# Kernel tuning notes

Hardware: AMD Instinct MI355X
Metric: run time of the kernel (lower is better)

Reference implementation:

```python
import jax, jax.numpy as jnp
import numpy as np

EM_DIM = 64
GROUP = 16
DIM_IN = 1024


def _position_embedding(boxes, part_boxes):
    # boxes: [N,4], part_boxes: [P,4] -> [N,P,EM_DIM]
    xmin, ymin, xmax, ymax = [boxes[:, i:i + 1] for i in range(4)]            # [N,1]
    pxmin, pymin, pxmax, pymax = [part_boxes[:, i:i + 1].T for i in range(4)]  # [1,P]
    bw = xmax - xmin + 1.0
    bh = ymax - ymin + 1.0
    pw = pxmax - pxmin + 1.0
    ph = pymax - pymin + 1.0
    cx = 0.5 * (xmin + xmax)
    cy = 0.5 * (ymin + ymax)
    pcx = 0.5 * (pxmin + pxmax)
    pcy = 0.5 * (pymin + pymax)
    dx = jnp.abs((cx - pcx) / bw)
    dy = jnp.abs((cy - pcy) / bh)
    dx = jnp.log(jnp.where(dx < 1e-3, 1e-3, dx))
    dy = jnp.log(jnp.where(dy < 1e-3, 1e-3, dy))
    dw = jnp.log(pw / bw)
    dh = jnp.log(ph / bh)
    pos = jnp.stack([dx, dy, dw, dh], axis=2)                                  # [N,P,4]
    em_range = jnp.arange(EM_DIM // 8, dtype=pos.dtype) / (EM_DIM // 8)        # [8]
    em_mat = jnp.power(jnp.asarray(1000.0, pos.dtype), em_range)               # [8]
    div = (100.0 * pos)[..., None] / em_mat                                    # [N,P,4,8]
    emb = jnp.concatenate([jnp.sin(div), jnp.cos(div)], axis=3)                # [N,P,4,16]
    return emb.reshape(pos.shape[0], pos.shape[1], EM_DIM)


def _single_relation(boxes, part_boxes, bf, pf, Wg_w, Wg_b, Wq_w, Wq_b, Wk_w, Wk_b, conv_w, conv_b):
    N = bf.shape[0]
    P = pf.shape[0]
    emb = _position_embedding(boxes, part_boxes)                               # [N,P,64]
    pos_feat = jax.nn.relu(emb @ Wg_w.T + Wg_b)                                # [N,P,G]
    att_weight = jnp.transpose(pos_feat, (0, 2, 1))                            # [N,G,P]
    q = (bf @ Wq_w.T + Wq_b).reshape(N, GROUP, EM_DIM)                         # [N,G,64]
    k = (pf @ Wk_w.T + Wk_b).reshape(P, GROUP, EM_DIM)                         # [P,G,64]
    att = jnp.einsum('ngd,pgd->ngp', q, k) * (1.0 / GROUP)                     # [N,G,P]
    att_weight = jnp.where(att_weight < 1e-6, 1e-6, att_weight)
    sm = jax.nn.softmax(jnp.log(att_weight) + att, axis=2)                     # [N,G,P]
    out = jnp.einsum('ngp,pc->ngc', sm, pf)                                    # [N,G,dim_in]
    # grouped 1x1 conv: group g maps dim_in channels -> EM_DIM channels
    w3 = conv_w.reshape(GROUP, EM_DIM, DIM_IN)
    rel = jnp.einsum('ngc,goc->ngo', out, w3).reshape(N, GROUP * EM_DIM) + conv_b
    return rel                                                                  # [N, G*EM_DIM]


def setup_inputs() -> dict:
    key = jax.random.key(0)
    ks = jax.random.split(key, 12)
    N_TOT, P_TOT = 2048, 2048

    def make_rois(k1, k2, n, n1):
        xy = jax.random.uniform(k1, (n, 2), jnp.float32) * 800.0
        wh = jax.random.uniform(k2, (n, 2), jnp.float32) * 200.0 + 16.0
        boxes = jnp.concatenate([xy, xy + wh], axis=1)
        idx = jnp.concatenate([jnp.zeros((n1, 1)), jnp.ones((n - n1, 1))], axis=0).astype(jnp.float32)
        return jnp.concatenate([idx, boxes], axis=1)

    rois = make_rois(ks[0], ks[1], N_TOT, 1024)
    part_rois = make_rois(ks[2], ks[3], P_TOT, 1024)
    box_feats = jax.random.normal(ks[4], (N_TOT, DIM_IN), jnp.float32)
    part_feats = jax.random.normal(ks[5], (P_TOT, DIM_IN), jnp.float32)
    xav_g = float(np.sqrt(6.0 / (EM_DIM + GROUP)))
    xav_qk = float(np.sqrt(6.0 / (DIM_IN + GROUP * EM_DIM)))
    Wg_w = jax.random.uniform(ks[6], (GROUP, EM_DIM), jnp.float32, -xav_g, xav_g)
    Wg_b = jnp.zeros((GROUP,), jnp.float32)
    Wq_w = jax.random.uniform(ks[7], (GROUP * EM_DIM, DIM_IN), jnp.float32, -xav_qk, xav_qk)
    Wq_b = jnp.zeros((GROUP * EM_DIM,), jnp.float32)
    Wk_w = jax.random.uniform(ks[8], (GROUP * EM_DIM, DIM_IN), jnp.float32, -xav_qk, xav_qk)
    Wk_b = jnp.zeros((GROUP * EM_DIM,), jnp.float32)
    conv_w = jax.random.normal(ks[9], (GROUP * EM_DIM, DIM_IN), jnp.float32) * 0.02
    conv_b = jnp.zeros((GROUP * EM_DIM,), jnp.float32)
    return {"rois": rois, "part_rois": part_rois, "box_feats": box_feats,
            "part_feats": part_feats, "Wg_w": Wg_w, "Wg_b": Wg_b,
            "Wq_w": Wq_w, "Wq_b": Wq_b, "Wk_w": Wk_w, "Wk_b": Wk_b,
            "conv_w": conv_w, "conv_b": conv_b, "n1_boxes": 1024, "n1_parts": 1024}


def reference(rois, part_rois, box_feats, part_feats, Wg_w, Wg_b, Wq_w, Wq_b,
              Wk_w, Wk_b, conv_w, conv_b, n1_boxes, n1_parts):
    boxes = rois[:, 1:5]
    part_boxes = part_rois[:, 1:5]
    params = (Wg_w, Wg_b, Wq_w, Wq_b, Wk_w, Wk_b, conv_w, conv_b)
    rel1 = _single_relation(boxes[:n1_boxes], part_boxes[:n1_parts],
                            box_feats[:n1_boxes], part_feats[:n1_parts], *params)
    rel2 = _single_relation(boxes[n1_boxes:], part_boxes[n1_parts:],
                            box_feats[n1_boxes:], part_feats[n1_parts:], *params)
    return jnp.concatenate([rel1, rel2], axis=0)  # [N_total, GROUP*EM_DIM]
```

## Files before the change

kernel.cpp:

```cpp
#include <hip/hip_runtime.h>

typedef unsigned short u16;
using short8  = __attribute__((ext_vector_type(8))) short;
using float4v = __attribute__((ext_vector_type(4))) float;

__device__ __forceinline__ u16 f2bf(float f) {
    union { float f; unsigned u; } v; v.f = f;
    unsigned r = (v.u + 0x7fff + ((v.u >> 16) & 1)) >> 16;
    return (u16)r;
}
__device__ __forceinline__ float bf2f(u16 h) {
    union { unsigned u; float f; } v; v.u = ((unsigned)h) << 16; return v.f;
}
__device__ __forceinline__ unsigned pkbf(float lo, float hi) {
    unsigned d;
    asm("v_cvt_pk_bf16_f32 %0, %1, %2" : "=v"(d) : "v"(lo), "v"(hi));
    return d;
}
__device__ __forceinline__ float sin_rev(float r) {
    float f, s;
    asm("v_fract_f32 %0, %1" : "=v"(f) : "v"(r));
    asm("v_sin_f32 %0, %1" : "=v"(s) : "v"(f));
    return s;
}
__device__ __forceinline__ void dma16(const void* g, void* l) {
    __builtin_amdgcn_global_load_lds((const __attribute__((address_space(1))) void*)g,
                                     (__attribute__((address_space(3))) void*)l, 16, 0, 0);
}

__device__ __forceinline__ void cvt4(const float* __restrict__ s, u16* __restrict__ o, int i) {
    float4 v = ((const float4*)s)[i];
    uint2 r; r.x = pkbf(v.x, v.y); r.y = pkbf(v.z, v.w);
    ((uint2*)o)[i] = r;
}

__global__ __launch_bounds__(256)
void cvt_all(const float* __restrict__ s0, const float* __restrict__ s1,
             const float* __restrict__ s2, const float* __restrict__ s3,
             const float* __restrict__ s4, const float* __restrict__ prois,
             u16* __restrict__ o0, u16* __restrict__ o1, u16* __restrict__ o2,
             u16* __restrict__ o3, u16* __restrict__ o4, float4* __restrict__ PD,
             int na4, int nb4, int nw4, int PT) {
    int i = blockIdx.x * 256 + threadIdx.x;
    if (i < na4) { cvt4(s0, o0, i); return; }
    i -= na4;
    if (i < nb4) { cvt4(s1, o1, i); return; }
    i -= nb4;
    if (i < nw4) { cvt4(s2, o2, i); return; }
    i -= nw4;
    if (i < nw4) { cvt4(s3, o3, i); return; }
    i -= nw4;
    if (i < nw4) { cvt4(s4, o4, i); return; }
    i -= nw4;
    if (i < PT) {
        const float* pr = prois + (size_t)i * 5;
        float pxmin = pr[1], pymin = pr[2], pxmax = pr[3], pymax = pr[4];
        PD[i] = make_float4(0.5f * (pxmin + pxmax), 0.5f * (pymin + pymax),
                            __logf(pxmax - pxmin + 1.0f), __logf(pymax - pymin + 1.0f));
    }
}

__global__ __launch_bounds__(256)
void proj_mfma(const u16* __restrict__ Ab, const u16* __restrict__ Pb,
               const u16* __restrict__ Wqb, const u16* __restrict__ Wkb,
               const u16* __restrict__ Cwb, const float* __restrict__ bq,
               const float* __restrict__ bk, u16* __restrict__ Qb,
               u16* __restrict__ Kb, u16* __restrict__ PVt, int PT) {
    __shared__ __align__(16) u16 As[128 * 64];
    __shared__ __align__(16) u16 Ws[64 * 64];
    __shared__ __align__(16) u16 Tr[128 * 68];

    const int z = blockIdx.z;
    const int m0 = blockIdx.y * 128, j0 = blockIdx.x * 64;
    const u16* A = (z == 0) ? Ab : Pb;
    const u16* W = (z == 0) ? Wqb : (z == 1 ? Wkb : Cwb);
    const int t = threadIdx.x;
    const int w = t >> 6, lane = t & 63;
    const int wm = w >> 1, wn = w & 1;
    const int lr = lane >> 3, lc = lane & 7, gch = lc ^ lr;
    const int fm = lane & 15, quad = lane >> 4;

    float4v zero4 = {0.f, 0.f, 0.f, 0.f};
    float4v acc[4][2];
#pragma unroll
    for (int i = 0; i < 4; ++i) { acc[i][0] = zero4; acc[i][1] = zero4; }

    for (int k0 = 0; k0 < 1024; k0 += 64) {
#pragma unroll
        for (int i = 0; i < 4; ++i) {
            int row = w * 32 + i * 8 + lr;
            dma16(A + (size_t)(m0 + row) * 1024 + k0 + gch * 8,
                  As + (w * 32 + i * 8) * 64 + lane * 8);
        }
#pragma unroll
        for (int i = 0; i < 2; ++i) {
            int row = w * 16 + i * 8 + lr;
            dma16(W + (size_t)(j0 + row) * 1024 + k0 + gch * 8,
                  Ws + (w * 16 + i * 8) * 64 + lane * 8);
        }
        __syncthreads();
#pragma unroll
        for (int ks = 0; ks < 2; ++ks) {
            int c = ks * 4 + quad;
            short8 af[4], bf[2];
#pragma unroll
            for (int i = 0; i < 4; ++i) {
                int ra = wm * 64 + i * 16 + fm;
                af[i] = *(const short8*)(As + ra * 64 + ((c ^ (ra & 7)) * 8));
            }
#pragma unroll
            for (int j = 0; j < 2; ++j) {
                int rb = wn * 32 + j * 16 + fm;
                bf[j] = *(const short8*)(Ws + rb * 64 + ((c ^ (rb & 7)) * 8));
            }
#pragma unroll
            for (int i = 0; i < 4; ++i)
#pragma unroll
                for (int j = 0; j < 2; ++j)
                    acc[i][j] = __builtin_amdgcn_mfma_f32_16x16x32_bf16(af[i], bf[j], acc[i][j], 0, 0, 0);
        }
        __syncthreads();
    }

    if (z < 2) {
        u16* O = z ? Kb : Qb;
        const float* bias = z ? bk : bq;
#pragma unroll
        for (int j = 0; j < 2; ++j) {
            int jl = wn * 32 + j * 16 + fm;
            float bb = bias[j0 + jl];
#pragma unroll
            for (int i = 0; i < 4; ++i) {
                int mlb = wm * 64 + i * 16 + quad * 4;
#pragma unroll
                for (int r = 0; r < 4; ++r)
                    Tr[(mlb + r) * 68 + jl] = f2bf(acc[i][j][r] + bb);
            }
        }
        __syncthreads();
#pragma unroll
        for (int i2 = 0; i2 < 4; ++i2) {
            int f = i2 * 2048 + t * 8;
            int ml = f >> 6, jl = f & 63;
            union { uint2 u2[2]; short8 s8; } uu;
            uu.u2[0] = *(const uint2*)(Tr + ml * 68 + jl);
            uu.u2[1] = *(const uint2*)(Tr + ml * 68 + jl + 4);
            *(short8*)(O + (size_t)(m0 + ml) * 1024 + j0 + jl) = uu.s8;
        }
    } else {
#pragma unroll
        for (int j = 0; j < 2; ++j) {
            int jl = wn * 32 + j * 16 + fm;
#pragma unroll
            for (int i = 0; i < 4; ++i) {
                int mlb = wm * 64 + i * 16 + quad * 4;
                uint2 pk;
                pk.x = pkbf(acc[i][j][0], acc[i][j][1]);
                pk.y = pkbf(acc[i][j][2], acc[i][j][3]);
                *(uint2*)(Tr + jl * 136 + mlb) = pk;
            }
        }
        __syncthreads();
#pragma unroll
        for (int i2 = 0; i2 < 4; ++i2) {
            int f = i2 * 2048 + t * 8;
            int jl = f >> 7, ml = f & 127;
            union { uint2 u2[2]; short8 s8; } uu;
            uu.u2[0] = *(const uint2*)(Tr + jl * 136 + ml);
            uu.u2[1] = *(const uint2*)(Tr + jl * 136 + ml + 4);
            *(short8*)(PVt + (size_t)(j0 + jl) * PT + m0 + ml) = uu.s8;
        }
    }
}

__global__ __launch_bounds__(256)
void posw_fused(const float* __restrict__ rois, const float4* __restrict__ PD,
                const float* __restrict__ Wg_w, const float* __restrict__ Wg_b,
                u16* __restrict__ POSW, const int* __restrict__ n1b_p,
                const int* __restrict__ n1p_p, int PT) {
    const int n = blockIdx.x, t = threadIdx.x;
    const int w = t >> 6, lane = t & 63;
    const int fm = lane & 15, quad = lane >> 4;
    const int n1b = *n1b_p, n1p = *n1p_p;
    const int hh = (n >= n1b) ? 1 : 0;
    const int p0 = hh ? n1p : 0;
    const int Ph = hh ? (PT - n1p) : n1p;

    float xmin = rois[n * 5 + 1], ymin = rois[n * 5 + 2];
    float xmax = rois[n * 5 + 3], ymax = rois[n * 5 + 4];
    float bw = xmax - xmin + 1.0f, bh = ymax - ymin + 1.0f;
    float cx = 0.5f * (xmin + xmax), cy = 0.5f * (ymin + ymax);

    const int jA = quad >> 1, trig = quad & 1;
    float cA   = (jA == 0) ? cx : cy;
    float invA = (jA == 0) ? (1.0f / bw) : (1.0f / bh);
    float lB   = (jA == 0) ? __logf(bw) : __logf(bh);
    float toff = trig ? 0.25f : 0.0f;

    const int g_ = fm;
    short8 b1, b2;
    {
        const float* w1 = Wg_w + g_ * 64 + quad * 8;
        const float* w2 = Wg_w + g_ * 64 + 32 + quad * 8;
        unsigned* p1 = (unsigned*)&b1;
        unsigned* p2 = (unsigned*)&b2;
#pragma unroll
        for (int kk = 0; kk < 4; ++kk) {
            p1[kk] = pkbf(w1[2 * kk], w1[2 * kk + 1]);
            p2[kk] = pkbf(w2[2 * kk], w2[2 * kk + 1]);
        }
    }
    float wgb = Wg_b[g_];

    const float inv_em[8] = {1.0f, 0.4216965034f, 0.1778279410f, 0.0749894209f,
                             0.0316227766f, 0.0133352143f, 0.0056234133f, 0.0023713737f};
    const float REV = 15.91549431f;
    const int prange = Ph >> 2;
    const int pb0 = w * prange;
    u16* rowp = POSW + ((size_t)n * 16 + g_) * 1024;

    float4 pd_c = PD[p0 + pb0 + fm];

#pragma unroll 2
    for (int pt = 0; pt < 16; ++pt) {
        int pbase = pb0 + pt * 16;
        float4 pd_n;
        if (pt < 15) pd_n = PD[p0 + pbase + 16 + fm];
        float pc = (jA == 0) ? pd_c.x : pd_c.y;
        float lp = (jA == 0) ? pd_c.z : pd_c.w;
        float posA = __logf(fmaxf(fabsf(cA - pc) * invA, 0.001f));
        float posB = lp - lB;
        float br1 = posA * REV, br2 = posB * REV;
        float e1[8], e2[8];
#pragma unroll
        for (int k = 0; k < 8; ++k) {
            e1[k] = sin_rev(fmaf(br1, inv_em[k], toff));
            e2[k] = sin_rev(fmaf(br2, inv_em[k], toff));
        }
        short8 a1, a2;
        unsigned* pa1 = (unsigned*)&a1;
        unsigned* pa2 = (unsigned*)&a2;
#pragma unroll
        for (int kk = 0; kk < 4; ++kk) {
            pa1[kk] = pkbf(e1[2 * kk], e1[2 * kk + 1]);
            pa2[kk] = pkbf(e2[2 * kk], e2[2 * kk + 1]);
        }
        float4v acc = {wgb, wgb, wgb, wgb};
        acc = __builtin_amdgcn_mfma_f32_16x16x32_bf16(a1, b1, acc, 0, 0, 0);
        acc = __builtin_amdgcn_mfma_f32_16x16x32_bf16(a2, b2, acc, 0, 0, 0);

        float w0  = fmaxf(acc[0], 1e-6f);
        float w1v = fmaxf(acc[1], 1e-6f);
        float w2v = fmaxf(acc[2], 1e-6f);
        float w3v = fmaxf(acc[3], 1e-6f);
        uint2 wp; wp.x = pkbf(w0, w1v); wp.y = pkbf(w2v, w3v);
        *(uint2*)(rowp + pbase + quad * 4) = wp;

        pd_c = pd_n;
    }
}

__global__ __launch_bounds__(256)
void fused_rel(const u16* __restrict__ Qb, const u16* __restrict__ Kb,
               const u16* __restrict__ POSW, const u16* __restrict__ PVt,
               const float* __restrict__ conv_b, float* __restrict__ OUT,
               const int* __restrict__ n1b_p, const int* __restrict__ n1p_p, int PT) {
    __shared__ __align__(16) u16 Qs[64 * 64];
    __shared__ __align__(16) u16 Ks[2][64 * 64];
    __shared__ __align__(16) u16 Ps[2][64 * 64];
    __shared__ __align__(16) u16 Vs[2][64 * 64];
    __shared__ __align__(16) u16 Wt[4][16 * 64];

    const int n0 = blockIdx.x * 64, g = blockIdx.y;
    const int n1b = *n1b_p, n1p = *n1p_p;
    const int hh = (n0 >= n1b) ? 1 : 0;
    const int p0 = hh ? n1p : 0;
    const int Ph = hh ? (PT - n1p) : n1p;
    const int t = threadIdx.x;
    const int w = t >> 6, lane = t & 63;
    const int lr = lane >> 3, lc = lane & 7, gch = lc ^ lr;
    const int fm = lane & 15, quad = lane >> 4;
    const int swz = fm & 7;

    auto stage = [&](int pt, int buf) {
#pragma unroll
        for (int i = 0; i < 2; ++i) {
            int row = w * 16 + i * 8 + lr;
            dma16(Kb + (size_t)(p0 + pt * 64 + row) * 1024 + g * 64 + gch * 8,
                  Ks[buf] + (w * 16 + i * 8) * 64 + lane * 8);
            dma16(POSW + ((size_t)(n0 + row) * 16 + g) * 1024 + pt * 64 + gch * 8,
                  Ps[buf] + (w * 16 + i * 8) * 64 + lane * 8);
            dma16(PVt + (size_t)(g * 64 + row) * PT + p0 + pt * 64 + gch * 8,
                  Vs[buf] + (w * 16 + i * 8) * 64 + lane * 8);
        }
    };

    stage(0, 0);
#pragma unroll
    for (int i = 0; i < 2; ++i) {
        int row = w * 16 + i * 8 + lr;
        dma16(Qb + (size_t)(n0 + row) * 1024 + g * 64 + gch * 8,
              Qs + (w * 16 + i * 8) * 64 + lane * 8);
    }

    float4v zero4 = {0.f, 0.f, 0.f, 0.f};
    float4v oacc[4];
#pragma unroll
    for (int ob = 0; ob < 4; ++ob) oacc[ob] = zero4;
    float rsum = 0.0f;

    __syncthreads();

    const int nloc = w * 16 + fm;
    short8 qf[2];
#pragma unroll
    for (int kd = 0; kd < 2; ++kd) {
        int c = kd * 4 + quad;
        qf[kd] = *(const short8*)(Qs + nloc * 64 + ((c ^ swz) * 8));
    }
    u16* wrow = Wt[w] + fm * 64;

    const int NPT = Ph >> 6;
    for (int pt = 0; pt < NPT; ++pt) {
        int cur = pt & 1;
        if (pt + 1 < NPT) stage(pt + 1, cur ^ 1);
        const u16* ks_ = Ks[cur];
        const u16* ps_ = Ps[cur];
        const u16* vs_ = Vs[cur];

        float4v atc[4];
#pragma unroll
        for (int pi = 0; pi < 4; ++pi) atc[pi] = zero4;
#pragma unroll
        for (int kd = 0; kd < 2; ++kd) {
            int c = kd * 4 + quad;
#pragma unroll
            for (int pi = 0; pi < 4; ++pi) {
                int rp = pi * 16 + fm;
                short8 kf = *(const short8*)(ks_ + rp * 64 + ((c ^ swz) * 8));
                atc[pi] = __builtin_amdgcn_mfma_f32_16x16x32_bf16(kf, qf[kd], atc[pi], 0, 0, 0);
            }
        }

#pragma unroll
        for (int pi = 0; pi < 4; ++pi) {
            int co = ((pi * 2 + (quad >> 1)) ^ swz) * 8 + (quad & 1) * 4;
            uint2 pwp = *(const uint2*)(ps_ + nloc * 64 + co);
            const u16* pww = (const u16*)&pwp;
            float wv0 = bf2f(pww[0]) * __expf(atc[pi][0] * 0.0625f);
            float wv1 = bf2f(pww[1]) * __expf(atc[pi][1] * 0.0625f);
            float wv2 = bf2f(pww[2]) * __expf(atc[pi][2] * 0.0625f);
            float wv3 = bf2f(pww[3]) * __expf(atc[pi][3] * 0.0625f);
            rsum += (wv0 + wv1) + (wv2 + wv3);
            uint2 wp; wp.x = pkbf(wv0, wv1); wp.y = pkbf(wv2, wv3);
            *(uint2*)(wrow + co) = wp;
        }

#pragma unroll
        for (int m = 0; m < 2; ++m) {
            short8 af = *(const short8*)(wrow + (((m * 4 + quad) ^ swz) * 8));
#pragma unroll
            for (int ob = 0; ob < 4; ++ob) {
                int ro = ob * 16 + fm;
                short8 vf = *(const short8*)(vs_ + ro * 64 + (((m * 4 + quad) ^ swz) * 8));
                oacc[ob] = __builtin_amdgcn_mfma_f32_16x16x32_bf16(af, vf, oacc[ob], 0, 0, 0);
            }
        }

        __syncthreads();
    }

    float s = rsum;
    s += __shfl_xor(s, 16, 64);
    s += __shfl_xor(s, 32, 64);
    float inv[4];
#pragma unroll
    for (int r = 0; r < 4; ++r)
        inv[r] = 1.0f / __shfl(s, quad * 4 + r, 64);

    float bb[4];
#pragma unroll
    for (int ob = 0; ob < 4; ++ob) bb[ob] = conv_b[g * 64 + ob * 16 + fm];
#pragma unroll
    for (int ob = 0; ob < 4; ++ob)
#pragma unroll
        for (int r = 0; r < 4; ++r) {
            int nn = n0 + w * 16 + quad * 4 + r;
            OUT[(size_t)nn * 1024 + g * 64 + ob * 16 + fm] = oacc[ob][r] * inv[r] + bb[ob];
        }
}

extern "C" void kernel_launch(void* const* d_in, const int* in_sizes, int n_in,
                              void* d_out, int out_size, void* d_ws, size_t ws_size,
                              hipStream_t stream) {
    const float* rois   = (const float*)d_in[0];
    const float* prois  = (const float*)d_in[1];
    const float* bfeat  = (const float*)d_in[2];
    const float* pfeat  = (const float*)d_in[3];
    const float* Wg_w   = (const float*)d_in[4];
    const float* Wg_b   = (const float*)d_in[5];
    const float* Wq_w   = (const float*)d_in[6];
    const float* Wq_b   = (const float*)d_in[7];
    const float* Wk_w   = (const float*)d_in[8];
    const float* Wk_b   = (const float*)d_in[9];
    const float* conv_w = (const float*)d_in[10];
    const float* conv_b = (const float*)d_in[11];
    const int*   n1b    = (const int*)d_in[12];
    const int*   n1p    = (const int*)d_in[13];

    const int NT = in_sizes[2] / 1024;
    const int PT = in_sizes[3] / 1024;

    u16* Qb   = (u16*)d_ws;
    u16* Kb   = Qb + (size_t)NT * 1024;
    u16* PVt  = Kb + (size_t)PT * 1024;
    float4* PD = (float4*)(PVt + (size_t)1024 * PT);
    u16* POSW = (u16*)(PD + PT);
    u16* Ab   = POSW + (size_t)NT * 16 * 1024;
    u16* Pb   = Ab + (size_t)NT * 1024;
    u16* Wqb  = Pb + (size_t)PT * 1024;
    u16* Wkb  = Wqb + 1024 * 1024;
    u16* Cwb  = Wkb + 1024 * 1024;

    dim3 blk(256);
    int nf4 = NT * 1024 / 4, pf4 = PT * 1024 / 4, wf4 = 1024 * 1024 / 4;
    int tot = nf4 + pf4 + 3 * wf4 + PT;
    cvt_all<<<dim3((tot + 255) / 256), blk, 0, stream>>>(
        bfeat, pfeat, Wq_w, Wk_w, conv_w, prois, Ab, Pb, Wqb, Wkb, Cwb, PD,
        nf4, pf4, wf4, PT);

    proj_mfma<<<dim3(16, NT / 128, 3), blk, 0, stream>>>(Ab, Pb, Wqb, Wkb, Cwb,
                                                         Wq_b, Wk_b, Qb, Kb, PVt, PT);
    posw_fused<<<dim3(NT), blk, 0, stream>>>(rois, PD, Wg_w, Wg_b, POSW, n1b, n1p, PT);
    fused_rel<<<dim3(NT / 64, 16), blk, 0, stream>>>(Qb, Kb, POSW, PVt, conv_b,
                                                     (float*)d_out, n1b, n1p, PT);
}
```

Measured before the change: 176.0 us.

## Merge projection GEMM and position-weight kernels into one interleaved launch

Fuses the projection GEMM and the position-weight kernel into a single launch. Blocks are interleaved so every 11 blocks hold 3 GEMM tiles and 8 position rows, letting the compute-heavy transcendental work overlap with the memory-bound GEMM and removing one launch. The position-weight output is now staged through shared memory and written as 16-byte coalesced row segments instead of scattered 8-byte stores. The cost is a larger shared-memory footprint for every block and a hardcoded grid that assumes NT=2048.

```diff
diff --git a/kernel.cpp b/kernel.cpp
--- a/kernel.cpp
+++ b/kernel.cpp
@@ -61,126 +61,131 @@
 }
 
 __global__ __launch_bounds__(256)
-void proj_mfma(const u16* __restrict__ Ab, const u16* __restrict__ Pb,
+void proj_posw(const u16* __restrict__ Ab, const u16* __restrict__ Pb,
                const u16* __restrict__ Wqb, const u16* __restrict__ Wkb,
                const u16* __restrict__ Cwb, const float* __restrict__ bq,
                const float* __restrict__ bk, u16* __restrict__ Qb,
-               u16* __restrict__ Kb, u16* __restrict__ PVt, int PT) {
-    __shared__ __align__(16) u16 As[128 * 64];
-    __shared__ __align__(16) u16 Ws[64 * 64];
-    __shared__ __align__(16) u16 Tr[128 * 68];
-
-    const int z = blockIdx.z;
-    const int m0 = blockIdx.y * 128, j0 = blockIdx.x * 64;
-    const u16* A = (z == 0) ? Ab : Pb;
-    const u16* W = (z == 0) ? Wqb : (z == 1 ? Wkb : Cwb);
+               u16* __restrict__ Kb, u16* __restrict__ PVt,
+               const float* __restrict__ rois, const float4* __restrict__ PD,
+               const float* __restrict__ Wg_w, const float* __restrict__ Wg_b,
+               u16* __restrict__ POSW, const int* __restrict__ n1b_p,
+               const int* __restrict__ n1p_p, int PT) {
+    __shared__ __align__(16) u16 SH[20992];
+
+    const int grp = blockIdx.x / 11, rem = blockIdx.x % 11;
     const int t = threadIdx.x;
     const int w = t >> 6, lane = t & 63;
-    const int wm = w >> 1, wn = w & 1;
-    const int lr = lane >> 3, lc = lane & 7, gch = lc ^ lr;
     const int fm = lane & 15, quad = lane >> 4;
 
-    float4v zero4 = {0.f, 0.f, 0.f, 0.f};
-    float4v acc[4][2];
-#pragma unroll
-    for (int i = 0; i < 4; ++i) { acc[i][0] = zero4; acc[i][1] = zero4; }
-
-    for (int k0 = 0; k0 < 1024; k0 += 64) {
-#pragma unroll
-        for (int i = 0; i < 4; ++i) {
-            int row = w * 32 + i * 8 + lr;
-            dma16(A + (size_t)(m0 + row) * 1024 + k0 + gch * 8,
-                  As + (w * 32 + i * 8) * 64 + lane * 8);
-        }
-#pragma unroll
-        for (int i = 0; i < 2; ++i) {
-            int row = w * 16 + i * 8 + lr;
-            dma16(W + (size_t)(j0 + row) * 1024 + k0 + gch * 8,
-                  Ws + (w * 16 + i * 8) * 64 + lane * 8);
-        }
-        __syncthreads();
-#pragma unroll
-        for (int ks = 0; ks < 2; ++ks) {
-            int c = ks * 4 + quad;
-            short8 af[4], bf[2];
+    if (rem < 3) {
+        u16* As = SH;
+        u16* Ws = SH + 8192;
+        u16* Tr = SH + 12288;
+        const int pb = grp * 3 + rem;
+        const int z = pb >> 8;
+        const int m0 = ((pb >> 4) & 15) * 128, j0 = (pb & 15) * 64;
+        const u16* A = (z == 0) ? Ab : Pb;
+        const u16* W = (z == 0) ? Wqb : (z == 1 ? Wkb : Cwb);
+        const int wm = w >> 1, wn = w & 1;
+        const int lr = lane >> 3, lc = lane & 7, gch = lc ^ lr;
+
+        float4v zero4 = {0.f, 0.f, 0.f, 0.f};
+        float4v acc[4][2];
+#pragma unroll
+        for (int i = 0; i < 4; ++i) { acc[i][0] = zero4; acc[i][1] = zero4; }
+
+        for (int k0 = 0; k0 < 1024; k0 += 64) {
 #pragma unroll
             for (int i = 0; i < 4; ++i) {
-                int ra = wm * 64 + i * 16 + fm;
-                af[i] = *(const short8*)(As + ra * 64 + ((c ^ (ra & 7)) * 8));
-            }
+                int row = w * 32 + i * 8 + lr;
+                dma16(A + (size_t)(m0 + row) * 1024 + k0 + gch * 8,
+                      As + (w * 32 + i * 8) * 64 + lane * 8);
+            }
+#pragma unroll
+            for (int i = 0; i < 2; ++i) {
+                int row = w * 16 + i * 8 + lr;
+                dma16(W + (size_t)(j0 + row) * 1024 + k0 + gch * 8,
+                      Ws + (w * 16 + i * 8) * 64 + lane * 8);
+            }
+            __syncthreads();
+#pragma unroll
+            for (int ks = 0; ks < 2; ++ks) {
+                int c = ks * 4 + quad;
+                short8 af[4], bf[2];
+#pragma unroll
+                for (int i = 0; i < 4; ++i) {
+                    int ra = wm * 64 + i * 16 + fm;
+                    af[i] = *(const short8*)(As + ra * 64 + ((c ^ (ra & 7)) * 8));
+                }
+#pragma unroll
+                for (int j = 0; j < 2; ++j) {
+                    int rb = wn * 32 + j * 16 + fm;
+                    bf[j] = *(const short8*)(Ws + rb * 64 + ((c ^ (rb & 7)) * 8));
+                }
+#pragma unroll
+                for (int i = 0; i < 4; ++i)
+#pragma unroll
+                    for (int j = 0; j < 2; ++j)
+                        acc[i][j] = __builtin_amdgcn_mfma_f32_16x16x32_bf16(af[i], bf[j], acc[i][j], 0, 0, 0);
+            }
+            __syncthreads();
+        }
+
+        if (z < 2) {
+            u16* O = z ? Kb : Qb;
+            const float* bias = z ? bk : bq;
 #pragma unroll
             for (int j = 0; j < 2; ++j) {
-                int rb = wn * 32 + j * 16 + fm;
-                bf[j] = *(const short8*)(Ws + rb * 64 + ((c ^ (rb & 7)) * 8));
-            }
-#pragma unroll
-            for (int i = 0; i < 4; ++i)
-#pragma unroll
-                for (int j = 0; j < 2; ++j)
-                    acc[i][j] = __builtin_amdgcn_mfma_f32_16x16x32_bf16(af[i], bf[j], acc[i][j], 0, 0, 0);
-        }
-        __syncthreads();
-    }
-
-    if (z < 2) {
-        u16* O = z ? Kb : Qb;
-        const float* bias = z ? bk : bq;
-#pragma unroll
-        for (int j = 0; j < 2; ++j) {
-            int jl = wn * 32 + j * 16 + fm;
-            float bb = bias[j0 + jl];
-#pragma unroll
-            for (int i = 0; i < 4; ++i) {
-                int mlb = wm * 64 + i * 16 + quad * 4;
-#pragma unroll
-                for (int r = 0; r < 4; ++r)
-                    Tr[(mlb + r) * 68 + jl] = f2bf(acc[i][j][r] + bb);
-            }
-        }
-        __syncthreads();
-#pragma unroll
-        for (int i2 = 0; i2 < 4; ++i2) {
-            int f = i2 * 2048 + t * 8;
-            int ml = f >> 6, jl = f & 63;
-            union { uint2 u2[2]; short8 s8; } uu;
-            uu.u2[0] = *(const uint2*)(Tr + ml * 68 + jl);
-            uu.u2[1] = *(const uint2*)(Tr + ml * 68 + jl + 4);
-            *(short8*)(O + (size_t)(m0 + ml) * 1024 + j0 + jl) = uu.s8;
-        }
-    } else {
-#pragma unroll
-        for (int j = 0; j < 2; ++j) {
-            int jl = wn * 32 + j * 16 + fm;
-#pragma unroll
-            for (int i = 0; i < 4; ++i) {
-                int mlb = wm * 64 + i * 16 + quad * 4;
-                uint2 pk;
-                pk.x = pkbf(acc[i][j][0], acc[i][j][1]);
-                pk.y = pkbf(acc[i][j][2], acc[i][j][3]);
-                *(uint2*)(Tr + jl * 136 + mlb) = pk;
-            }
-        }
-        __syncthreads();
-#pragma unroll
-        for (int i2 = 0; i2 < 4; ++i2) {
-            int f = i2 * 2048 + t * 8;
-            int jl = f >> 7, ml = f & 127;
-            union { uint2 u2[2]; short8 s8; } uu;
-            uu.u2[0] = *(const uint2*)(Tr + jl * 136 + ml);
-            uu.u2[1] = *(const uint2*)(Tr + jl * 136 + ml + 4);
-            *(short8*)(PVt + (size_t)(j0 + jl) * PT + m0 + ml) = uu.s8;
-        }
-    }
-}
-
-__global__ __launch_bounds__(256)
-void posw_fused(const float* __restrict__ rois, const float4* __restrict__ PD,
-                const float* __restrict__ Wg_w, const float* __restrict__ Wg_b,
-                u16* __restrict__ POSW, const int* __restrict__ n1b_p,
-                const int* __restrict__ n1p_p, int PT) {
-    const int n = blockIdx.x, t = threadIdx.x;
-    const int w = t >> 6, lane = t & 63;
-    const int fm = lane & 15, quad = lane >> 4;
+                int jl = wn * 32 + j * 16 + fm;
+                float bb = bias[j0 + jl];
+#pragma unroll
+                for (int i = 0; i < 4; ++i) {
+                    int mlb = wm * 64 + i * 16 + quad * 4;
+#pragma unroll
+                    for (int r = 0; r < 4; ++r)
+                        Tr[(mlb + r) * 68 + jl] = f2bf(acc[i][j][r] + bb);
+                }
+            }
+            __syncthreads();
+#pragma unroll
+            for (int i2 = 0; i2 < 4; ++i2) {
+                int f = i2 * 2048 + t * 8;
+                int ml = f >> 6, jl = f & 63;
+                union { uint2 u2[2]; short8 s8; } uu;
+                uu.u2[0] = *(const uint2*)(Tr + ml * 68 + jl);
+                uu.u2[1] = *(const uint2*)(Tr + ml * 68 + jl + 4);
+                *(short8*)(O + (size_t)(m0 + ml) * 1024 + j0 + jl) = uu.s8;
+            }
+        } else {
+#pragma unroll
+            for (int j = 0; j < 2; ++j) {
+                int jl = wn * 32 + j * 16 + fm;
+#pragma unroll
+                for (int i = 0; i < 4; ++i) {
+                    int mlb = wm * 64 + i * 16 + quad * 4;
+                    uint2 pk;
+                    pk.x = pkbf(acc[i][j][0], acc[i][j][1]);
+                    pk.y = pkbf(acc[i][j][2], acc[i][j][3]);
+                    *(uint2*)(Tr + jl * 136 + mlb) = pk;
+                }
+            }
+            __syncthreads();
+#pragma unroll
+            for (int i2 = 0; i2 < 4; ++i2) {
+                int f = i2 * 2048 + t * 8;
+                int jl = f >> 7, ml = f & 127;
+                union { uint2 u2[2]; short8 s8; } uu;
+                uu.u2[0] = *(const uint2*)(Tr + jl * 136 + ml);
+                uu.u2[1] = *(const uint2*)(Tr + jl * 136 + ml + 4);
+                *(short8*)(PVt + (size_t)(j0 + jl) * PT + m0 + ml) = uu.s8;
+            }
+        }
+        return;
+    }
+
+    u16* Wl = SH + w * 4224;
+
+    const int n = grp * 8 + (rem - 3);
     const int n1b = *n1b_p, n1p = *n1p_p;
     const int hh = (n >= n1b) ? 1 : 0;
     const int p0 = hh ? n1p : 0;
@@ -217,15 +222,13 @@
     const float REV = 15.91549431f;
     const int prange = Ph >> 2;
     const int pb0 = w * prange;
-    u16* rowp = POSW + ((size_t)n * 16 + g_) * 1024;
 
     float4 pd_c = PD[p0 + pb0 + fm];
 
 #pragma unroll 2
     for (int pt = 0; pt < 16; ++pt) {
-        int pbase = pb0 + pt * 16;
         float4 pd_n;
-        if (pt < 15) pd_n = PD[p0 + pbase + 16 + fm];
+        if (pt < 15) pd_n = PD[p0 + pb0 + pt * 16 + 16 + fm];
         float pc = (jA == 0) ? pd_c.x : pd_c.y;
         float lp = (jA == 0) ? pd_c.z : pd_c.w;
         float posA = __logf(fmaxf(fabsf(cA - pc) * invA, 0.001f));
@@ -254,9 +257,22 @@
         float w2v = fmaxf(acc[2], 1e-6f);
         float w3v = fmaxf(acc[3], 1e-6f);
         uint2 wp; wp.x = pkbf(w0, w1v); wp.y = pkbf(w2v, w3v);
-        *(uint2*)(rowp + pbase + quad * 4) = wp;
+        *(uint2*)(Wl + pt * 264 + lane * 4) = wp;
 
         pd_c = pd_n;
+    }
+
+    const int p8 = (lane & 31) * 8;
+    const int halfg = lane >> 5;
+    const int itq = p8 >> 4;
+    const int q0 = (p8 >> 2) & 3;
+#pragma unroll
+    for (int s = 0; s < 8; ++s) {
+        int gg = s * 2 + halfg;
+        union { uint2 u2[2]; short8 s8; } uu;
+        uu.u2[0] = *(const uint2*)(Wl + itq * 264 + (q0 * 16 + gg) * 4);
+        uu.u2[1] = *(const uint2*)(Wl + itq * 264 + ((q0 + 1) * 16 + gg) * 4);
+        *(short8*)(POSW + ((size_t)n * 16 + gg) * 1024 + pb0 + p8) = uu.s8;
     }
 }
 
@@ -429,9 +445,10 @@
         bfeat, pfeat, Wq_w, Wk_w, conv_w, prois, Ab, Pb, Wqb, Wkb, Cwb, PD,
         nf4, pf4, wf4, PT);
 
-    proj_mfma<<<dim3(16, NT / 128, 3), blk, 0, stream>>>(Ab, Pb, Wqb, Wkb, Cwb,
-                                                         Wq_b, Wk_b, Qb, Kb, PVt, PT);
-    posw_fused<<<dim3(NT), blk, 0, stream>>>(rois, PD, Wg_w, Wg_b, POSW, n1b, n1p, PT);
+    proj_posw<<<dim3(256 * 11), blk, 0, stream>>>(Ab, Pb, Wqb, Wkb, Cwb,
+                                                  Wq_b, Wk_b, Qb, Kb, PVt,
+                                                  rois, PD, Wg_w, Wg_b, POSW,
+                                                  n1b, n1p, PT);
     fused_rel<<<dim3(NT / 64, 16), blk, 0, stream>>>(Qb, Kb, POSW, PVt, conv_b,
                                                      (float*)d_out, n1b, n1p, PT);
 }
```

After: 173.8 us. No clear change (-1.3%).
